# Performance work log

Measured on AMD Instinct MI355X. Metric: run time of the kernel, lower is better.

The kernel has to match this reference:

```python
import jax, jax.numpy as jnp
import numpy as np

LIMIT_A = -0.1  # hard-concrete stretch lower limit
LIMIT_B = 1.1   # hard-concrete stretch upper limit
BATCH, IN_F, OUT_F = 64, 1024, 1024


def setup_inputs() -> dict:
    key = jax.random.key(0)
    kx, kw, kq = jax.random.split(key, 3)
    # fuzzy truth values in [0, 1]
    x = jax.random.uniform(kx, (BATCH, IN_F), dtype=jnp.float32)
    # Parameter(0.1 * torch.rand(in_features, out_features))
    weights = 0.1 * jax.random.uniform(kw, (IN_F, OUT_F), dtype=jnp.float32)
    # qz_loga init: normal(log(1-droprate)-log(droprate), 0.01) with droprate_init=0.5 -> mean 0
    qz_loga = 0.01 * jax.random.normal(kq, (IN_F,), dtype=jnp.float32)
    return {"x": x, "weights": weights, "qz_loga\u200b".replace("\u200b", ""): qz_loga}


def reference(x, weights, qz_loga):
    # Eval-mode L0ConjunctionLayer.forward (group_l0=True, randomly_binarize=False):
    #   z = hardtanh(sigmoid(qz_loga) * (limit_b - limit_a) + limit_a, 0, 1)  # (in,)
    #   w = z[:, None] * weights                                             # (in, out)
    #   out = prod_i (1 - (1 - x)[:, :, None] * w[None, :, :])               # (batch, out)
    pi = jax.nn.sigmoid(qz_loga)
    z = jnp.clip(pi * (LIMIT_B - LIMIT_A) + LIMIT_A, 0.0, 1.0)
    w = z[:, None] * weights  # (in, out)
    # fuzzy-AND gate: broadcast multiply then product-reduce over in_features
    out = jnp.prod(1.0 - (1.0 - x)[:, :, None] * w[None, :, :], axis=1)
    return out
```

## Files before the change

### kernel.cpp

```cpp
#include <hip/hip_runtime.h>


#define BATCH 64
#define IN_F  1024
#define OUT_F 1024

__global__ __launch_bounds__(256) void l0_fuzzy_and_main(
        const float* __restrict__ x,
        const float* __restrict__ w,
        const float* __restrict__ qz,
        float* __restrict__ outp,
        int L)
{
    extern __shared__ float u_lds[];
    const int bg = blockIdx.x;
    const int s  = blockIdx.y;
    const int i0 = s * L;
    const int b0 = bg * 4;
    const int t  = threadIdx.x;

    for (int idx = t; idx < L * 4; idx += 256) {
        const int ii = idx >> 2;
        const int bb = idx & 3;
        const int gi = i0 + ii;
        const float q  = qz[gi];
        const float pi = 1.0f / (1.0f + expf(-q));
        float z = fmaf(pi, 1.2f, -0.1f);
        z = fminf(fmaxf(z, 0.0f), 1.0f);
        const float xv = x[(b0 + bb) * IN_F + gi];
        u_lds[idx] = (1.0f - xv) * z;
    }
    __syncthreads();

    const int o = t * 4;
    float acc[4][4];
#pragma unroll
    for (int bb = 0; bb < 4; ++bb)
#pragma unroll
        for (int j = 0; j < 4; ++j)
            acc[bb][j] = 1.0f;

    const float* wp = w + (size_t)i0 * OUT_F + o;
#pragma unroll 8
    for (int ii = 0; ii < L; ++ii) {
        const float4 w4 = *(const float4*)wp;
        wp += OUT_F;
        const float4 u4 = *(const float4*)(&u_lds[ii * 4]);
        const float wv[4] = {w4.x, w4.y, w4.z, w4.w};
        const float uv[4] = {u4.x, u4.y, u4.z, u4.w};
#pragma unroll
        for (int bb = 0; bb < 4; ++bb)
#pragma unroll
            for (int j = 0; j < 4; ++j)
                acc[bb][j] *= fmaf(-uv[bb], wv[j], 1.0f);
    }

    float* op = outp + (size_t)(s * BATCH + b0) * OUT_F + o;
#pragma unroll
    for (int bb = 0; bb < 4; ++bb) {
        float4 v = make_float4(acc[bb][0], acc[bb][1], acc[bb][2], acc[bb][3]);
        *(float4*)(op + (size_t)bb * OUT_F) = v;
    }
}

__global__ __launch_bounds__(256) void l0_combine(
        const float* __restrict__ part, float* __restrict__ out, int S)
{
    const int idx = blockIdx.x * 256 + threadIdx.x;
    float p = 1.0f;
#pragma unroll 8
    for (int s = 0; s < S; ++s)
        p *= part[(size_t)s * (BATCH * OUT_F) + idx];
    out[idx] = p;
}

extern "C" void kernel_launch(void* const* d_in, const int* in_sizes, int n_in,
                              void* d_out, int out_size, void* d_ws, size_t ws_size,
                              hipStream_t stream)
{
    const float* x  = (const float*)d_in[0];
    const float* w  = (const float*)d_in[1];
    const float* qz = (const float*)d_in[2];
    float* out = (float*)d_out;

    int S = 32;
    while (S > 1 && (size_t)S * BATCH * OUT_F * sizeof(float) > ws_size)
        S >>= 1;
    const int L = IN_F / S;

    float* target = (S > 1) ? (float*)d_ws : out;
    dim3 grid(BATCH / 4, S);
    size_t lds_bytes = (size_t)L * 4 * sizeof(float);
    hipLaunchKernelGGL(l0_fuzzy_and_main, grid, dim3(256), lds_bytes, stream,
                       x, w, qz, target, L);

    if (S > 1) {
        hipLaunchKernelGGL(l0_combine, dim3((BATCH * OUT_F) / 256), dim3(256),
                           0, stream, (const float*)d_ws, out, S);
    }
}
```

Baseline: 77.31 us.

## Fuse split-K partial products into one kernel with in-block LDS reduction

Replaces the two-kernel split-K scheme (partials written to workspace, then a combine kernel) with a single kernel. Each block handles 32 outputs by 4 batch rows over the full input dimension, splitting IN_F across 32 thread groups and reducing the partial products through LDS. This removes the workspace round trip and the second launch. In exchange every block recomputes the sigmoid gates and the x-derived terms for all 1024 inputs, and each block reads narrower 128-byte strips of the weights.

```diff
diff --git a/kernel.cpp b/kernel.cpp
--- a/kernel.cpp
+++ b/kernel.cpp
@@ -1,38 +1,47 @@
 #include <hip/hip_runtime.h>
 
 
-#define BATCH 64
 #define IN_F  1024
 #define OUT_F 1024
+#define BATCH 64
 
-__global__ __launch_bounds__(256) void l0_fuzzy_and_main(
+#define U_WORDS    4224
+#define ZP_WORDS   4608
+
+__global__ __launch_bounds__(256) void l0_fuzzy_and_fused(
         const float* __restrict__ x,
         const float* __restrict__ w,
         const float* __restrict__ qz,
-        float* __restrict__ outp,
-        int L)
+        float* __restrict__ out)
 {
-    extern __shared__ float u_lds[];
-    const int bg = blockIdx.x;
-    const int s  = blockIdx.y;
-    const int i0 = s * L;
+    __shared__ float lds[U_WORDS + ZP_WORDS];
+    float* u  = lds;
+    float* zp = lds + U_WORDS;
+
+    const int t  = threadIdx.x;
+    const int og = blockIdx.x;
+    const int bg = blockIdx.y;
     const int b0 = bg * 4;
-    const int t  = threadIdx.x;
 
-    for (int idx = t; idx < L * 4; idx += 256) {
-        const int ii = idx >> 2;
-        const int bb = idx & 3;
-        const int gi = i0 + ii;
-        const float q  = qz[gi];
+    for (int i = t; i < IN_F; i += 256) {
+        const float q  = qz[i];
         const float pi = 1.0f / (1.0f + expf(-q));
-        float z = fmaf(pi, 1.2f, -0.1f);
-        z = fminf(fmaxf(z, 0.0f), 1.0f);
-        const float xv = x[(b0 + bb) * IN_F + gi];
-        u_lds[idx] = (1.0f - xv) * z;
+        zp[i] = fminf(fmaxf(fmaf(pi, 1.2f, -0.1f), 0.0f), 1.0f);
     }
     __syncthreads();
 
-    const int o = t * 4;
+    for (int idx = t; idx < IN_F * 4; idx += 256) {
+        const int i  = idx & (IN_F - 1);
+        const int bb = idx >> 10;
+        const float uv = (1.0f - x[(size_t)(b0 + bb) * IN_F + i]) * zp[i];
+        u[(i >> 5) * 132 + (i & 31) * 4 + bb] = uv;
+    }
+    __syncthreads();
+
+    const int ot = t & 7;
+    const int ch = t >> 3;
+    const int o0 = og * 32 + ot * 4;
+
     float acc[4][4];
 #pragma unroll
     for (int bb = 0; bb < 4; ++bb)
@@ -40,12 +49,13 @@
         for (int j = 0; j < 4; ++j)
             acc[bb][j] = 1.0f;
 
-    const float* wp = w + (size_t)i0 * OUT_F + o;
+    const float* wp = w + (size_t)(ch * 32) * OUT_F + o0;
+    const float* up = u + ch * 132;
 #pragma unroll 8
-    for (int ii = 0; ii < L; ++ii) {
+    for (int ii = 0; ii < 32; ++ii) {
         const float4 w4 = *(const float4*)wp;
         wp += OUT_F;
-        const float4 u4 = *(const float4*)(&u_lds[ii * 4]);
+        const float4 u4 = *(const float4*)(up + ii * 4);
         const float wv[4] = {w4.x, w4.y, w4.z, w4.w};
         const float uv[4] = {u4.x, u4.y, u4.z, u4.w};
 #pragma unroll
@@ -55,23 +65,25 @@
                 acc[bb][j] *= fmaf(-uv[bb], wv[j], 1.0f);
     }
 
-    float* op = outp + (size_t)(s * BATCH + b0) * OUT_F + o;
 #pragma unroll
-    for (int bb = 0; bb < 4; ++bb) {
-        float4 v = make_float4(acc[bb][0], acc[bb][1], acc[bb][2], acc[bb][3]);
-        *(float4*)(op + (size_t)bb * OUT_F) = v;
+    for (int bb = 0; bb < 4; ++bb)
+#pragma unroll
+        for (int j = 0; j < 4; ++j)
+            zp[(bb * 32 + ot * 4 + j) * 36 + ch] = acc[bb][j];
+    __syncthreads();
+
+    if (t < 128) {
+        const int bb = t >> 5;
+        const int ol = t & 31;
+        const float* pp = zp + t * 36;
+        float prod = 1.0f;
+#pragma unroll
+        for (int c = 0; c < 32; c += 4) {
+            const float4 v = *(const float4*)(pp + c);
+            prod *= v.x * v.y * v.z * v.w;
+        }
+        out[(size_t)(b0 + bb) * OUT_F + og * 32 + ol] = prod;
     }
-}
-
-__global__ __launch_bounds__(256) void l0_combine(
-        const float* __restrict__ part, float* __restrict__ out, int S)
-{
-    const int idx = blockIdx.x * 256 + threadIdx.x;
-    float p = 1.0f;
-#pragma unroll 8
-    for (int s = 0; s < S; ++s)
-        p *= part[(size_t)s * (BATCH * OUT_F) + idx];
-    out[idx] = p;
 }
 
 extern "C" void kernel_launch(void* const* d_in, const int* in_sizes, int n_in,
@@ -83,19 +95,7 @@
     const float* qz = (const float*)d_in[2];
     float* out = (float*)d_out;
 
-    int S = 32;
-    while (S > 1 && (size_t)S * BATCH * OUT_F * sizeof(float) > ws_size)
-        S >>= 1;
-    const int L = IN_F / S;
-
-    float* target = (S > 1) ? (float*)d_ws : out;
-    dim3 grid(BATCH / 4, S);
-    size_t lds_bytes = (size_t)L * 4 * sizeof(float);
-    hipLaunchKernelGGL(l0_fuzzy_and_main, grid, dim3(256), lds_bytes, stream,
-                       x, w, qz, target, L);
-
-    if (S > 1) {
-        hipLaunchKernelGGL(l0_combine, dim3((BATCH * OUT_F) / 256), dim3(256),
-                           0, stream, (const float*)d_ws, out, S);
-    }
+    dim3 grid(OUT_F / 32, BATCH / 4);
+    hipLaunchKernelGGL(l0_fuzzy_and_fused, grid, dim3(256), 0, stream,
+                       x, w, qz, out);
 }
```

Result: faster. 74.43 us (-3.7%).
